# Performance work log

Measured on AMD Instinct MI355X. Metric: run time of the kernel, lower is better.

Reference implementation:

```python
import jax, jax.numpy as jnp
import numpy as np

N_NODES = 100000
N_EDGES = 1600000
IN, HID, OUT = 64, 64, 32


def setup_inputs() -> dict:
    key = jax.random.key(0)
    ks = jax.random.split(key, 8)
    x = jax.random.normal(ks[0], (N_NODES, IN), dtype=jnp.float32)
    src = jax.random.randint(ks[1], (N_EDGES,), 0, N_NODES)
    dst = jax.random.randint(ks[2], (N_EDGES,), 0, N_NODES)
    s = 0.05
    return {
        "x": x,
        "src": src,
        "dst": dst,
        "W_self1": jax.random.normal(ks[3], (IN, HID), dtype=jnp.float32) * s,
        "W_neigh1": jax.random.normal(ks[4], (IN, HID), dtype=jnp.float32) * s,
        "b1": jnp.zeros((HID,), dtype=jnp.float32),
        "W_self2": jax.random.normal(ks[5], (HID, OUT), dtype=jnp.float32) * s,
        "W_neigh2": jax.random.normal(ks[6], (HID, OUT), dtype=jnp.float32) * s,
        "b2": jnp.zeros((OUT,), dtype=jnp.float32),
    }


def reference(x, src, dst, W_self1, W_neigh1, b1, W_self2, W_neigh2, b2):
    n = x.shape[0]
    # in-degree per destination node; mean reducer yields 0 for isolated nodes
    deg = jax.ops.segment_sum(jnp.ones_like(dst, dtype=x.dtype), dst, num_segments=n)
    denom = jnp.maximum(deg, 1.0)[:, None]  # [N, 1]

    def sage_conv(h, W_self, W_neigh, b):
        # gather src features, sum into dst, divide by in-degree -> mean aggregation
        agg = jax.ops.segment_sum(h[src], dst, num_segments=n) / denom  # [N, F]
        return h @ W_self + agg @ W_neigh + b

    h = jax.nn.relu(sage_conv(x, W_self1, W_neigh1, b1))
    return sage_conv(h, W_self2, W_neigh2, b2)
```

## Files before the change

### kernel.cpp

```cpp
#include <hip/hip_runtime.h>

#define NF 64
#define OF 32

#define NPB 512
#define NPB_SHIFT 9
#define BCAP 12288
#define BIN_CHUNK 4096

typedef unsigned int uint;
typedef unsigned short ushort;
typedef __attribute__((ext_vector_type(8))) short bf16x8;
typedef __attribute__((ext_vector_type(4))) float f32x4;


__device__ __forceinline__ ushort f2bf(float f) {
    uint u = __float_as_uint(f);
    uint r = (u + 0x7fffu + ((u >> 16) & 1u)) >> 16;
    return (ushort)r;
}
__device__ __forceinline__ float bf2f(ushort b) { return __uint_as_float(((uint)b) << 16); }
__device__ __forceinline__ float blo(uint u) { return __uint_as_float(u << 16); }
__device__ __forceinline__ float bhi(uint u) { return __uint_as_float(u & 0xffff0000u); }


__global__ __launch_bounds__(256) void binning_kernel(
        const int* __restrict__ src, const int* __restrict__ dst, int n_edges,
        int* __restrict__ gcur, uint* __restrict__ stage) {
    __shared__ int hist[256];
    __shared__ int base[256];
    __shared__ int rank[256];
    int t = threadIdx.x;
    hist[t] = 0;
    rank[t] = 0;
    __syncthreads();

    int e0 = blockIdx.x * BIN_CHUNK;
    uint my_pack[16];
    int my_b[16];
#pragma unroll
    for (int j = 0; j < 16; j++) {
        int e = e0 + j * 256 + t;
        if (e < n_edges) {
            int s = src[e];
            int d = dst[e];
            int b = d >> NPB_SHIFT;
            my_b[j] = b;
            my_pack[j] = ((uint)(d & (NPB - 1)) << 17) | (uint)s;
            atomicAdd(&hist[b], 1);
        } else {
            my_b[j] = -1;
        }
    }
    __syncthreads();
    if (hist[t] > 0) base[t] = atomicAdd(&gcur[t], hist[t]);
    __syncthreads();
#pragma unroll
    for (int j = 0; j < 16; j++) {
        if (my_b[j] >= 0) {
            int r = atomicAdd(&rank[my_b[j]], 1);
            int pos = base[my_b[j]] + r;
            if (pos < BCAP) stage[(size_t)my_b[j] * BCAP + pos] = my_pack[j];
        }
    }
}

__global__ __launch_bounds__(256) void build_kernel(
        const uint* __restrict__ stage, const int* __restrict__ gcnt,
        int* __restrict__ row_ptr, int* __restrict__ csr, int n, int nb) {
    __shared__ int bsc[256];
    __shared__ int ncnt[NPB];
    __shared__ int lcur[NPB];
    __shared__ int psum[256];
    __shared__ int lcsr[BCAP];

    int b = blockIdx.x;
    int t = threadIdx.x;

    bsc[t] = (t < nb) ? gcnt[t] : 0;
    __syncthreads();
    for (int off = 1; off < 256; off <<= 1) {
        int u = (t >= off) ? bsc[t - off] : 0;
        __syncthreads();
        bsc[t] += u;
        __syncthreads();
    }
    int gbase = (b == 0) ? 0 : bsc[b - 1];

    int cnt = min(gcnt[b], BCAP);
    int node0 = b << NPB_SHIFT;
    const uint* st = stage + (size_t)b * BCAP;

    ncnt[t] = 0;
    ncnt[t + 256] = 0;
    __syncthreads();
    for (int i = t; i < cnt; i += 256)
        atomicAdd(&ncnt[st[i] >> 17], 1);
    __syncthreads();

    int a0 = ncnt[2 * t], a1 = ncnt[2 * t + 1];
    psum[t] = a0 + a1;
    __syncthreads();
    for (int off = 1; off < 256; off <<= 1) {
        int u = (t >= off) ? psum[t - off] : 0;
        __syncthreads();
        psum[t] += u;
        __syncthreads();
    }
    int excl = (t == 0) ? 0 : psum[t - 1];
    int off0 = excl, off1 = excl + a0;
    int g0 = node0 + 2 * t, g1 = node0 + 2 * t + 1;
    if (g0 < n) row_ptr[g0] = gbase + off0;
    if (g1 < n) row_ptr[g1] = gbase + off1;
    lcur[2 * t] = off0;
    lcur[2 * t + 1] = off1;
    __syncthreads();

    for (int i = t; i < cnt; i += 256) {
        uint p = st[i];
        int slot = atomicAdd(&lcur[p >> 17], 1);
        lcsr[slot] = (int)(p & 0x1FFFFu);
    }
    __syncthreads();
    for (int i = t; i < cnt; i += 256)
        csr[gbase + i] = lcsr[i];

    if (b == nb - 1 && t == 0) row_ptr[n] = bsc[nb - 1];
}


__global__ void convert_prep_kernel(const float* __restrict__ in, ushort* __restrict__ out, int n4,
                                    const float* __restrict__ Ws1, const float* __restrict__ Wn1,
                                    const float* __restrict__ Ws2, const float* __restrict__ Wn2,
                                    ushort* __restrict__ wt1, ushort* __restrict__ wt2,
                                    int* __restrict__ gcur) {
    int i = blockIdx.x * blockDim.x + threadIdx.x;
    if (blockIdx.x == 0) gcur[threadIdx.x] = 0;
    if (i < n4) {
        float4 v = *(const float4*)(in + (size_t)i * 4);
        ushort4 o;
        o.x = f2bf(v.x); o.y = f2bf(v.y); o.z = f2bf(v.z); o.w = f2bf(v.w);
        *(ushort4*)(out + (size_t)i * 4) = o;
    }
    if (i < NF * 128) {
        int c = i >> 7, k = i & 127;
        float v = (k < 64) ? Ws1[k * NF + c] : Wn1[(k - 64) * NF + c];
        wt1[i] = f2bf(v);
    }
    if (i < OF * 128) {
        int c = i >> 7, k = i & 127;
        float v = (k < 64) ? Ws2[k * OF + c] : Wn2[(k - 64) * OF + c];
        wt2[i] = f2bf(v);
    }
}


template<int FW>
__global__ __launch_bounds__(256) void gather_kernel(
        const ushort* __restrict__ feat,
        const int* __restrict__ row_ptr, const int* __restrict__ csr,
        ushort* __restrict__ agg, int n) {
    constexpr int LPG = FW / 8;
    constexpr int NPW = 64 / LPG;
    int lane = threadIdx.x & 63;
    int g = lane / LPG;
    int fo = (lane % LPG) * 8;
    int wave = blockIdx.x * 4 + (threadIdx.x >> 6);
    int stride = gridDim.x * 4 * NPW;

    for (int n0 = wave * NPW + g; n0 < n; n0 += stride) {
        int beg = row_ptr[n0], end = row_ptr[n0 + 1];
        int cnt = end - beg;
        int full = beg + (cnt & ~7);
        float a0 = 0.f, a1 = 0.f, a2 = 0.f, a3 = 0.f;
        float a4 = 0.f, a5 = 0.f, a6 = 0.f, a7 = 0.f;
        for (int o = beg; o < full; o += 8) {
            uint4 v[8];
#pragma unroll
            for (int j = 0; j < 8; j++)
                v[j] = *(const uint4*)(feat + (size_t)csr[o + j] * FW + fo);
#pragma unroll
            for (int j = 0; j < 8; j++) {
                a0 += blo(v[j].x); a1 += bhi(v[j].x);
                a2 += blo(v[j].y); a3 += bhi(v[j].y);
                a4 += blo(v[j].z); a5 += bhi(v[j].z);
                a6 += blo(v[j].w); a7 += bhi(v[j].w);
            }
        }
        if (full < end) {
            uint4 v[8];
#pragma unroll
            for (int j = 0; j < 8; j++) {
                int e = min(full + j, end - 1);
                v[j] = *(const uint4*)(feat + (size_t)csr[e] * FW + fo);
            }
#pragma unroll
            for (int j = 0; j < 8; j++) {
                bool ok = (full + j) < end;
                uint vx = ok ? v[j].x : 0u, vy = ok ? v[j].y : 0u;
                uint vz = ok ? v[j].z : 0u, vw = ok ? v[j].w : 0u;
                a0 += blo(vx); a1 += bhi(vx);
                a2 += blo(vy); a3 += bhi(vy);
                a4 += blo(vz); a5 += bhi(vz);
                a6 += blo(vw); a7 += bhi(vw);
            }
        }
        float inv = 1.0f / (float)max(cnt, 1);
        uint4 o4;
        o4.x = (uint)f2bf(a0 * inv) | ((uint)f2bf(a1 * inv) << 16);
        o4.y = (uint)f2bf(a2 * inv) | ((uint)f2bf(a3 * inv) << 16);
        o4.z = (uint)f2bf(a4 * inv) | ((uint)f2bf(a5 * inv) << 16);
        o4.w = (uint)f2bf(a6 * inv) | ((uint)f2bf(a7 * inv) << 16);
        *(uint4*)(agg + (size_t)n0 * FW + fo) = o4;
    }
}


__global__ __launch_bounds__(256) void gemm1_fused_kernel(
        const ushort* __restrict__ xb, const ushort* __restrict__ aggx,
        const ushort* __restrict__ wt1,
        const ushort* __restrict__ wt2,
        const float* __restrict__ b1,
        ushort* __restrict__ hb, ushort* __restrict__ un2, int n, int ntiles) {
    __shared__ char tiles[4][2048];
    int lane = threadIdx.x & 63;
    int wslot = threadIdx.x >> 6;
    char* tile = tiles[wslot];
    int col = lane & 15, kg = lane >> 4;
    int wid = blockIdx.x * 4 + wslot;
    int nw = gridDim.x * 4;
    int sw = (col & 7) << 4;

    bf16x8 wfrag[4][4];
#pragma unroll
    for (int ct = 0; ct < 4; ct++)
#pragma unroll
        for (int kt = 0; kt < 4; kt++)
            wfrag[ct][kt] = *(const bf16x8*)(wt1 + ((ct * 16 + col) * 128 + kt * 32 + kg * 8));
    bf16x8 wn2frag[2][2];
#pragma unroll
    for (int c2 = 0; c2 < 2; c2++)
#pragma unroll
        for (int kt = 0; kt < 2; kt++)
            wn2frag[c2][kt] = *(const bf16x8*)(wt2 + ((c2 * 16 + col) * 128 + 64 + kt * 32 + kg * 8));
    float4 bias4[4];
#pragma unroll
    for (int ct = 0; ct < 4; ct++) bias4[ct] = *(const float4*)(b1 + ct * 16 + kg * 4);

    for (int t = wid; t < ntiles; t += nw) {
        int r0 = t * 16;
        int row = min(r0 + col, n - 1);
        const ushort* xrow = xb + (size_t)row * NF;
        const ushort* arow = aggx + (size_t)row * NF;
        bf16x8 nfrag[4];
        nfrag[0] = *(const bf16x8*)(xrow + kg * 8);
        nfrag[1] = *(const bf16x8*)(xrow + 32 + kg * 8);
        nfrag[2] = *(const bf16x8*)(arow + kg * 8);
        nfrag[3] = *(const bf16x8*)(arow + 32 + kg * 8);

        int node = r0 + col;
        bool ok = node < n;
#pragma unroll
        for (int ct = 0; ct < 4; ct++) {
            f32x4 c = {0.f, 0.f, 0.f, 0.f};
#pragma unroll
            for (int kt = 0; kt < 4; kt++)
                c = __builtin_amdgcn_mfma_f32_16x16x32_bf16(wfrag[ct][kt], nfrag[kt], c, 0, 0, 0);
            uint2 pk;
            pk.x = (uint)f2bf(fmaxf(c[0] + bias4[ct].x, 0.f))
                 | ((uint)f2bf(fmaxf(c[1] + bias4[ct].y, 0.f)) << 16);
            pk.y = (uint)f2bf(fmaxf(c[2] + bias4[ct].z, 0.f))
                 | ((uint)f2bf(fmaxf(c[3] + bias4[ct].w, 0.f)) << 16);
            *(uint2*)(tile + col * 128 + ((ct * 32 + kg * 8) ^ sw)) = pk;
            if (ok) *(uint2*)(hb + (size_t)node * NF + ct * 16 + kg * 4) = pk;
        }

        bf16x8 hfrag[2];
        hfrag[0] = *(const bf16x8*)(tile + col * 128 + ((0 * 64 + kg * 16) ^ sw));
        hfrag[1] = *(const bf16x8*)(tile + col * 128 + ((1 * 64 + kg * 16) ^ sw));
#pragma unroll
        for (int c2 = 0; c2 < 2; c2++) {
            f32x4 c = {0.f, 0.f, 0.f, 0.f};
            c = __builtin_amdgcn_mfma_f32_16x16x32_bf16(wn2frag[c2][0], hfrag[0], c, 0, 0, 0);
            c = __builtin_amdgcn_mfma_f32_16x16x32_bf16(wn2frag[c2][1], hfrag[1], c, 0, 0, 0);
            if (ok) {
                uint2 pk;
                pk.x = (uint)f2bf(c[0]) | ((uint)f2bf(c[1]) << 16);
                pk.y = (uint)f2bf(c[2]) | ((uint)f2bf(c[3]) << 16);
                *(uint2*)(un2 + (size_t)node * OF + c2 * 16 + kg * 4) = pk;
            }
        }
    }
}


__global__ __launch_bounds__(256) void gemm2_kernel(
        const ushort* __restrict__ hb, const ushort* __restrict__ aggu,
        const ushort* __restrict__ wt2,
        const float* __restrict__ b2,
        float* __restrict__ out, int n, int ntiles) {
    int lane = threadIdx.x & 63;
    int col = lane & 15, kg = lane >> 4;
    int wid = blockIdx.x * 4 + (threadIdx.x >> 6);
    int nw = gridDim.x * 4;

    bf16x8 wfrag[2][2];
#pragma unroll
    for (int ct = 0; ct < 2; ct++)
#pragma unroll
        for (int kt = 0; kt < 2; kt++)
            wfrag[ct][kt] = *(const bf16x8*)(wt2 + ((ct * 16 + col) * 128 + kt * 32 + kg * 8));
    float4 bias4[2];
#pragma unroll
    for (int ct = 0; ct < 2; ct++) bias4[ct] = *(const float4*)(b2 + ct * 16 + kg * 4);

    for (int t = wid; t < ntiles; t += nw) {
        int r0 = t * 16;
        int row = min(r0 + col, n - 1);
        const ushort* hrow = hb + (size_t)row * NF;
        bf16x8 nfrag[2];
        nfrag[0] = *(const bf16x8*)(hrow + kg * 8);
        nfrag[1] = *(const bf16x8*)(hrow + 32 + kg * 8);

        int node = r0 + col;
        bool ok = node < n;
#pragma unroll
        for (int ct = 0; ct < 2; ct++) {
            f32x4 c = {0.f, 0.f, 0.f, 0.f};
            c = __builtin_amdgcn_mfma_f32_16x16x32_bf16(wfrag[ct][0], nfrag[0], c, 0, 0, 0);
            c = __builtin_amdgcn_mfma_f32_16x16x32_bf16(wfrag[ct][1], nfrag[1], c, 0, 0, 0);
            if (ok) {
                uint2 au = *(const uint2*)(aggu + (size_t)node * OF + ct * 16 + kg * 4);
                float4 o;
                o.x = c[0] + bias4[ct].x + blo(au.x);
                o.y = c[1] + bias4[ct].y + bhi(au.x);
                o.z = c[2] + bias4[ct].z + blo(au.y);
                o.w = c[3] + bias4[ct].w + bhi(au.y);
                *(float4*)(out + (size_t)node * OF + ct * 16 + kg * 4) = o;
            }
        }
    }
}


extern "C" void kernel_launch(void* const* d_in, const int* in_sizes, int n_in,
                              void* d_out, int out_size, void* d_ws, size_t ws_size,
                              hipStream_t stream) {
    const float* x   = (const float*)d_in[0];
    const int*   src = (const int*)d_in[1];
    const int*   dst = (const int*)d_in[2];
    const float* Ws1 = (const float*)d_in[3];
    const float* Wn1 = (const float*)d_in[4];
    const float* b1  = (const float*)d_in[5];
    const float* Ws2 = (const float*)d_in[6];
    const float* Wn2 = (const float*)d_in[7];
    const float* b2  = (const float*)d_in[8];
    float* out = (float*)d_out;

    int n_nodes = in_sizes[0] / NF;
    int n_edges = in_sizes[1];
    int nb = (n_nodes + NPB - 1) >> NPB_SHIFT;

    auto align4k = [](size_t v) { return (v + 4095) & ~(size_t)4095; };
    char* ws = (char*)d_ws;
    size_t gcur_b = align4k(256 * 4);
    size_t rp_b   = align4k(((size_t)n_nodes + 1) * 4);
    size_t csr_b  = align4k((size_t)n_edges * 4);
    size_t xb_b   = align4k((size_t)n_nodes * NF * 2);
    size_t hb_b   = xb_b;
    size_t agg_b  = xb_b;
    size_t un2_b  = align4k((size_t)n_nodes * OF * 2);
    int* gcur        = (int*)ws;
    int* row_ptr     = (int*)(ws + gcur_b);
    int* csr         = (int*)(ws + gcur_b + rp_b);
    ushort* xb       = (ushort*)(ws + gcur_b + rp_b + csr_b);
    ushort* hb       = (ushort*)(ws + gcur_b + rp_b + csr_b + xb_b);
    ushort* agg      = (ushort*)(ws + gcur_b + rp_b + csr_b + xb_b + hb_b);
    uint*   stage    = (uint*)agg;
    ushort* aggu     = agg;
    ushort* un2      = (ushort*)(ws + gcur_b + rp_b + csr_b + xb_b + hb_b + agg_b);
    ushort* wt1      = (ushort*)(ws + gcur_b + rp_b + csr_b + xb_b + hb_b + agg_b + un2_b);
    ushort* wt2      = wt1 + NF * 128;

    int bin_blocks = (n_edges + BIN_CHUNK - 1) / BIN_CHUNK;
    int n4      = n_nodes * NF / 4;
    int cblocks = (n4 + 255) / 256;
    int ntiles  = (n_nodes + 15) / 16;
    int mblocks = 512;

    convert_prep_kernel<<<cblocks, 256, 0, stream>>>(x, xb, n4, Ws1, Wn1, Ws2, Wn2, wt1, wt2, gcur);
    binning_kernel<<<bin_blocks, 256, 0, stream>>>(src, dst, n_edges, gcur, stage);
    build_kernel<<<nb, 256, 0, stream>>>(stage, gcur, row_ptr, csr, n_nodes, nb);

    gather_kernel<64><<<1024, 256, 0, stream>>>(xb, row_ptr, csr, agg, n_nodes);
    gemm1_fused_kernel<<<mblocks, 256, 0, stream>>>(xb, agg, wt1, wt2, b1, hb, un2, n_nodes, ntiles);

    gather_kernel<32><<<512, 256, 0, stream>>>(un2, row_ptr, csr, aggu, n_nodes);
    gemm2_kernel<<<mblocks, 256, 0, stream>>>(hb, aggu, wt2, b2, out, n_nodes, ntiles);
}
```

Before: 122.2 us.

## Locally sort edges by bucket in LDS before coalesced stage writes

The binning kernel now loads 16 contiguous edges per thread with vector loads. It counting-sorts them by destination bucket in shared memory using a prefix scan, then writes the staged entries out so that consecutive threads hit consecutive addresses within each bucket. This replaces scattered per-edge global writes with mostly contiguous runs. Both gather kernels also get twice as many blocks. The change adds about 20KB of LDS per binning block and several extra barriers, which may lower occupancy.

After: 115.5 us (median of 2 runs). 1.06x faster.

```diff
diff --git a/kernel.cpp b/kernel.cpp
--- a/kernel.cpp
+++ b/kernel.cpp
@@ -28,40 +28,70 @@
         const int* __restrict__ src, const int* __restrict__ dst, int n_edges,
         int* __restrict__ gcur, uint* __restrict__ stage) {
     __shared__ int hist[256];
-    __shared__ int base[256];
-    __shared__ int rank[256];
+    __shared__ int lofs[256];
+    __shared__ int gbase[256];
+    __shared__ int lrank[256];
+    __shared__ uint lsorted[BIN_CHUNK];
+    __shared__ unsigned char lbkt[BIN_CHUNK];
+
     int t = threadIdx.x;
     hist[t] = 0;
-    rank[t] = 0;
+    lrank[t] = 0;
     __syncthreads();
 
     int e0 = blockIdx.x * BIN_CHUNK;
-    uint my_pack[16];
-    int my_b[16];
-#pragma unroll
-    for (int j = 0; j < 16; j++) {
-        int e = e0 + j * 256 + t;
-        if (e < n_edges) {
-            int s = src[e];
-            int d = dst[e];
-            int b = d >> NPB_SHIFT;
-            my_b[j] = b;
-            my_pack[j] = ((uint)(d & (NPB - 1)) << 17) | (uint)s;
-            atomicAdd(&hist[b], 1);
-        } else {
-            my_b[j] = -1;
-        }
-    }
-    __syncthreads();
-    if (hist[t] > 0) base[t] = atomicAdd(&gcur[t], hist[t]);
-    __syncthreads();
-#pragma unroll
-    for (int j = 0; j < 16; j++) {
-        if (my_b[j] >= 0) {
-            int r = atomicAdd(&rank[my_b[j]], 1);
-            int pos = base[my_b[j]] + r;
-            if (pos < BCAP) stage[(size_t)my_b[j] * BCAP + pos] = my_pack[j];
-        }
+    int base_e = e0 + t * 16;
+    int nloc = min(16, max(0, n_edges - base_e));
+
+    uint es[16], ed[16];
+    if (nloc == 16) {
+#pragma unroll
+        for (int q = 0; q < 4; q++) {
+            uint4 s4 = *(const uint4*)(src + base_e + q * 4);
+            uint4 d4 = *(const uint4*)(dst + base_e + q * 4);
+            es[q * 4 + 0] = s4.x; es[q * 4 + 1] = s4.y; es[q * 4 + 2] = s4.z; es[q * 4 + 3] = s4.w;
+            ed[q * 4 + 0] = d4.x; ed[q * 4 + 1] = d4.y; ed[q * 4 + 2] = d4.z; ed[q * 4 + 3] = d4.w;
+        }
+    } else {
+        for (int j = 0; j < nloc; j++) {
+            es[j] = (uint)src[base_e + j];
+            ed[j] = (uint)dst[base_e + j];
+        }
+    }
+
+    for (int j = 0; j < nloc; j++)
+        atomicAdd(&hist[ed[j] >> NPB_SHIFT], 1);
+    __syncthreads();
+
+    int hv = hist[t];
+    lofs[t] = hv;
+    __syncthreads();
+    for (int off = 1; off < 256; off <<= 1) {
+        int u = (t >= off) ? lofs[t - off] : 0;
+        __syncthreads();
+        lofs[t] += u;
+        __syncthreads();
+    }
+    int incl = lofs[t];
+    __syncthreads();
+    lofs[t] = incl - hv;
+    if (hv > 0) gbase[t] = atomicAdd(&gcur[t], hv);
+    __syncthreads();
+
+    for (int j = 0; j < nloc; j++) {
+        int b = ed[j] >> NPB_SHIFT;
+        int r = atomicAdd(&lrank[b], 1);
+        int pos = lofs[b] + r;
+        lsorted[pos] = ((ed[j] & (NPB - 1)) << 17) | es[j];
+        lbkt[pos] = (unsigned char)b;
+    }
+    __syncthreads();
+
+    int bcnt = min(BIN_CHUNK, n_edges - e0);
+    for (int i = t; i < bcnt; i += 256) {
+        int b = lbkt[i];
+        int pos = gbase[b] + (i - lofs[b]);
+        if (pos < BCAP) stage[(size_t)b * BCAP + pos] = lsorted[i];
     }
 }
 
@@ -392,9 +422,9 @@
     binning_kernel<<<bin_blocks, 256, 0, stream>>>(src, dst, n_edges, gcur, stage);
     build_kernel<<<nb, 256, 0, stream>>>(stage, gcur, row_ptr, csr, n_nodes, nb);
 
-    gather_kernel<64><<<1024, 256, 0, stream>>>(xb, row_ptr, csr, agg, n_nodes);
+    gather_kernel<64><<<2048, 256, 0, stream>>>(xb, row_ptr, csr, agg, n_nodes);
     gemm1_fused_kernel<<<mblocks, 256, 0, stream>>>(xb, agg, wt1, wt2, b1, hb, un2, n_nodes, ntiles);
 
-    gather_kernel<32><<<512, 256, 0, stream>>>(un2, row_ptr, csr, aggu, n_nodes);
+    gather_kernel<32><<<1024, 256, 0, stream>>>(un2, row_ptr, csr, aggu, n_nodes);
     gemm2_kernel<<<mblocks, 256, 0, stream>>>(hb, aggu, wt2, b2, out, n_nodes, ntiles);
 }
```
